# Kernel tuning notes

Hardware: AMD Instinct MI355X
Metric: run time of the kernel (lower is better)

## Reference

```python
import jax, jax.numpy as jnp
import numpy as np

TAU = 100.0
EPS = 1e-6

def _norm(a):
    n = jnp.linalg.norm(a, axis=-1, keepdims=True)
    return a / jnp.maximum(n, EPS)

def setup_inputs() -> dict:
    key = jax.random.key(0)
    k1, k2, k3 = jax.random.split(key, 3)
    A, T, B, V, D = 64, 32, 64, 12, 512
    text_feat = jax.random.normal(k1, (A, T, D), dtype=jnp.float32)
    video_feat = jax.random.normal(k2, (B, V, D), dtype=jnp.float32)
    text_mask = jax.random.randint(k3, (A, T), 0, 2, dtype=jnp.int32)
    # guarantee at least one valid token per text so masked softmaxes are finite
    text_mask = text_mask.at[:, 0].set(1)
    return {"text_feat": text_feat, "video_feat": video_feat, "text_mask": text_mask}

def reference(text_feat, video_feat, text_mask):
    tm = text_mask.astype(text_feat.dtype)          # [A,T]
    t = _norm(text_feat)                            # [A,T,D]
    v = _norm(video_feat)                           # [B,V,D]
    neg_inf = jnp.asarray(-jnp.inf, t.dtype)

    logits = jnp.einsum('atd,bvd->abtv', t, v)      # [A,B,T,V]
    logits = logits * tm[:, None, :, None]          # zero out masked text tokens

    # video-side softmax over frames v, then aggregate video into text space
    vps1 = jax.nn.softmax(logits * TAU, axis=-1)            # [A,B,T,V]
    tf1 = jnp.einsum('abtv,bvd->abtd', vps1, v)             # [A,B,T,D]  (largest intermediate)
    t2v = jnp.einsum('abtd,atd->abt', tf1, t)               # [A,B,T]

    # text-side masked softmax over tokens t, aggregate text into video space
    tps1 = jax.nn.softmax(jnp.where(logits == 0, neg_inf, logits) * TAU, axis=-2)
    vf1 = jnp.einsum('abtv,atd->abvd', tps1, t)             # [A,B,V,D]
    v2t = jnp.einsum('abvd,bvd->abv', vf1, v)               # [A,B,V]

    tps2 = jax.nn.softmax(jnp.where(t2v == 0, neg_inf, t2v) * TAU, axis=-1)
    vf2 = jnp.einsum('abt,atd->abd', tps2, t)               # [A,B,D]
    vps2 = jax.nn.softmax(v2t * TAU, axis=-1)
    tf2 = jnp.einsum('abv,bvd->abd', vps2, v)               # [A,B,D]

    return jnp.einsum('abd,abd->ab', vf2, tf2)              # [A,B]
```

## Files before the change

kernel.cpp:

```cpp
#include <hip/hip_runtime.h>
#include <math.h>

#define A_ 64
#define T_ 32
#define B_ 64
#define V_ 12
#define D_ 512
#define TAUF 100.0f
#define NCH 8

#define AHI 0
#define ALO 8192
#define BHI 16384
#define BLO 22528
#define BUFBYTES 28672

typedef __attribute__((ext_vector_type(8))) short bf16x8;
typedef __attribute__((ext_vector_type(4))) float f32x4;

__device__ __forceinline__ void splitT(const float4 x0, const float4 x1,
                                       bf16x8& hv, bf16x8& lv, float& ss)
{
    float y[8] = {x0.x, x0.y, x0.z, x0.w, x1.x, x1.y, x1.z, x1.w};
    #pragma unroll
    for (int j = 0; j < 8; ++j) {
        ss += y[j] * y[j];
        unsigned int u = __float_as_uint(y[j]);
        float hf = __uint_as_float(u & 0xffff0000u);
        hv[j] = (short)(u >> 16);
        lv[j] = (short)(__float_as_uint(y[j] - hf) >> 16);
    }
}

__global__ __launch_bounds__(256)
void fused_kernel(const float* __restrict__ text,
                  const float* __restrict__ video,
                  const int* __restrict__ mask,
                  float* __restrict__ out)
{
    const int wgid = blockIdx.x;
    const int xcd  = wgid & 7;
    const int i    = wgid >> 3;
    const int bm   = xcd * 4 + (i >> 4);
    const int bn   = i & 15;
    const int tid  = threadIdx.x;
    const int wid  = tid >> 6;
    const int lane = tid & 63;
    const int r16  = lane & 15;
    const int kg4  = lane >> 4;

    __shared__ __align__(16) char stage[2][BUFBYTES];
    __shared__ float nrmA[8][64];
    __shared__ float nrmB[8][48];
    __shared__ float invA[64];
    __shared__ float invB[48];
    __shared__ int   msh[2][T_];
    __shared__ float v2t_sh[8][V_];
    __shared__ float wv_sh[8][V_];
    __shared__ float stats1[8];

    if (tid < 64) msh[tid >> 5][tid & 31] = mask[(bm * 2 + (tid >> 5)) * T_ + (tid & 31)];

    const int arow0 = tid >> 3, akg = tid & 7;
    const int arow1 = arow0 + 32;
    const float* asrc0 = text + ((size_t)(bm * 64 + arow0)) * D_ + akg * 8;
    const float* asrc1 = text + ((size_t)(bm * 64 + arow1)) * D_ + akg * 8;
    const int brow0 = tid >> 3, bkg = tid & 7;
    const int brow1 = brow0 + 24;
    const float* bsrc0 = video + ((size_t)(bn * 48 + brow0)) * D_ + bkg * 8;
    const float* bsrc1 = video + ((size_t)(bn * 48 + brow1)) * D_ + bkg * 8;

    const int adst0 = (akg * 64 + (arow0 ^ akg)) * 16;
    const int adst1 = (akg * 64 + (arow1 ^ akg)) * 16;
    const int bdst0 = BHI + (bkg * 48 + (brow0 ^ bkg)) * 16;
    const int bdst1 = BHI + (bkg * 48 + (brow1 ^ bkg)) * 16;

    float ssA0 = 0.f, ssA1 = 0.f, ssB0 = 0.f, ssB1 = 0.f;

    auto PACK = [&](int bufi, int k) {
        char* buf = stage[bufi];
        {
            const float4* s = (const float4*)(asrc0 + k * 64);
            bf16x8 hv, lv;
            splitT(s[0], s[1], hv, lv, ssA0);
            *(bf16x8*)(buf + adst0)       = hv;
            *(bf16x8*)(buf + ALO + adst0) = lv;
        }
        {
            const float4* s = (const float4*)(asrc1 + k * 64);
            bf16x8 hv, lv;
            splitT(s[0], s[1], hv, lv, ssA1);
            *(bf16x8*)(buf + adst1)       = hv;
            *(bf16x8*)(buf + ALO + adst1) = lv;
        }
        if (tid < 192) {
            {
                const float4* s = (const float4*)(bsrc0 + k * 64);
                bf16x8 hv, lv;
                splitT(s[0], s[1], hv, lv, ssB0);
                *(bf16x8*)(buf + bdst0)             = hv;
                *(bf16x8*)(buf + (BLO - BHI) + bdst0) = lv;
            }
            {
                const float4* s = (const float4*)(bsrc1 + k * 64);
                bf16x8 hv, lv;
                splitT(s[0], s[1], hv, lv, ssB1);
                *(bf16x8*)(buf + bdst1)             = hv;
                *(bf16x8*)(buf + (BLO - BHI) + bdst1) = lv;
            }
        }
    };

    const int rowa = wid * 16 + r16;
    int aoff[2], boff[2][3];
    #pragma unroll
    for (int s = 0; s < 2; ++s) {
        int kg = s * 4 + kg4;
        aoff[s] = (kg * 64 + (rowa ^ kg)) * 16;
        #pragma unroll
        for (int c = 0; c < 3; ++c) {
            int rowb = c * 16 + r16;
            boff[s][c] = BHI + (kg * 48 + (rowb ^ kg)) * 16;
        }
    }

    f32x4 acc0 = {0.f, 0.f, 0.f, 0.f};
    f32x4 acc1 = {0.f, 0.f, 0.f, 0.f};
    f32x4 acc2 = {0.f, 0.f, 0.f, 0.f};

    PACK(0, 0);
    __syncthreads();

    #pragma unroll 2
    for (int k = 0; k < NCH; ++k) {
        if (k + 1 < NCH) PACK((k + 1) & 1, k + 1);
        const char* buf = stage[k & 1];
        #pragma unroll
        for (int s = 0; s < 2; ++s) {
            bf16x8 aH  = *(const bf16x8*)(buf + aoff[s]);
            bf16x8 aL  = *(const bf16x8*)(buf + ALO + aoff[s]);
            bf16x8 bH0 = *(const bf16x8*)(buf + boff[s][0]);
            bf16x8 bL0 = *(const bf16x8*)(buf + (BLO - BHI) + boff[s][0]);
            bf16x8 bH1 = *(const bf16x8*)(buf + boff[s][1]);
            bf16x8 bL1 = *(const bf16x8*)(buf + (BLO - BHI) + boff[s][1]);
            bf16x8 bH2 = *(const bf16x8*)(buf + boff[s][2]);
            bf16x8 bL2 = *(const bf16x8*)(buf + (BLO - BHI) + boff[s][2]);
            acc0 = __builtin_amdgcn_mfma_f32_16x16x32_bf16(aH, bH0, acc0, 0, 0, 0);
            acc1 = __builtin_amdgcn_mfma_f32_16x16x32_bf16(aH, bH1, acc1, 0, 0, 0);
            acc2 = __builtin_amdgcn_mfma_f32_16x16x32_bf16(aH, bH2, acc2, 0, 0, 0);
            acc0 = __builtin_amdgcn_mfma_f32_16x16x32_bf16(aH, bL0, acc0, 0, 0, 0);
            acc1 = __builtin_amdgcn_mfma_f32_16x16x32_bf16(aH, bL1, acc1, 0, 0, 0);
            acc2 = __builtin_amdgcn_mfma_f32_16x16x32_bf16(aH, bL2, acc2, 0, 0, 0);
            acc0 = __builtin_amdgcn_mfma_f32_16x16x32_bf16(aL, bH0, acc0, 0, 0, 0);
            acc1 = __builtin_amdgcn_mfma_f32_16x16x32_bf16(aL, bH1, acc1, 0, 0, 0);
            acc2 = __builtin_amdgcn_mfma_f32_16x16x32_bf16(aL, bH2, acc2, 0, 0, 0);
        }
        __syncthreads();
    }

    nrmA[akg][arow0] = ssA0;
    nrmA[akg][arow1] = ssA1;
    if (tid < 192) { nrmB[bkg][brow0] = ssB0; nrmB[bkg][brow1] = ssB1; }
    __syncthreads();
    if (tid < 64) {
        float s = 0.f;
        #pragma unroll
        for (int j = 0; j < 8; ++j) s += nrmA[j][tid];
        invA[tid] = 1.0f / fmaxf(sqrtf(s), 1e-6f);
    } else if (tid < 112) {
        int r = tid - 64;
        float s = 0.f;
        #pragma unroll
        for (int j = 0; j < 8; ++j) s += nrmB[j][r];
        invB[r] = 1.0f / fmaxf(sqrtf(s), 1e-6f);
    }
    __syncthreads();

    float* Lf = (float*)&stage[0][0];
    {
        #pragma unroll
        for (int r = 0; r < 4; ++r) {
            int Mrow0 = wid * 16 + kg4 * 4 + r;
            int al = Mrow0 >> 5, t = Mrow0 & 31;
            float ia = invA[Mrow0];
            int c0 = r16, c1 = 16 + r16, c2 = 32 + r16;
            int bl0 = c0 / 12, bl1 = c1 / 12, bl2 = c2 / 12;
            Lf[((al * 4 + bl0) * T_ + t) * V_ + (c0 - bl0 * 12)] = acc0[r] * ia * invB[c0];
            Lf[((al * 4 + bl1) * T_ + t) * V_ + (c1 - bl1 * 12)] = acc1[r] * ia * invB[c1];
            Lf[((al * 4 + bl2) * T_ + t) * V_ + (c2 - bl2 * 12)] = acc2[r] * ia * invB[c2];
        }
    }
    __syncthreads();

    const int p   = tid >> 5;
    const int l32 = tid & 31;
    const int al  = p >> 2, bl = p & 3;
    const float* Lrow = &Lf[((al * 4 + bl) * T_ + l32) * V_];

    float t2v_val;
    {
        float l[V_];
        #pragma unroll
        for (int j = 0; j < V_; ++j) l[j] = Lrow[j];
        if (msh[al][l32]) {
            float m = -1e30f;
            #pragma unroll
            for (int j = 0; j < V_; ++j) m = fmaxf(m, l[j]);
            float s = 0.f, num = 0.f;
            #pragma unroll
            for (int j = 0; j < V_; ++j) {
                float e = expf(TAUF * (l[j] - m));
                s += e; num += e * l[j];
            }
            t2v_val = num / s;
        } else {
            float s = 0.f;
            #pragma unroll
            for (int j = 0; j < V_; ++j) s += l[j];
            t2v_val = s * (1.0f / V_);
        }
    }

    bool  ex = (t2v_val == 0.0f);
    float xm = ex ? -1e30f : t2v_val;
    #pragma unroll
    for (int m = 16; m >= 1; m >>= 1) xm = fmaxf(xm, __shfl_xor(xm, m, 32));
    float w2 = ex ? 0.0f : expf(TAUF * (t2v_val - xm));
    float W2 = w2;
    #pragma unroll
    for (int m = 16; m >= 1; m >>= 1) W2 += __shfl_xor(W2, m, 32);

    if (l32 < V_) {
        float m = -1e30f;
        for (int j = 0; j < T_; ++j) {
            float Lraw = Lf[((al * 4 + bl) * T_ + j) * V_ + l32];
            float Lm = msh[al][j] ? Lraw : 0.0f;
            if (Lm != 0.0f) m = fmaxf(m, Lm);
        }
        float s = 0.f, num = 0.f;
        for (int j = 0; j < T_; ++j) {
            float Lraw = Lf[((al * 4 + bl) * T_ + j) * V_ + l32];
            float Lm = msh[al][j] ? Lraw : 0.0f;
            if (Lm != 0.0f) {
                float e = expf(TAUF * (Lm - m));
                s += e; num += e * Lraw;
            }
        }
        v2t_sh[p][l32] = num / s;
    }
    __syncthreads();

    if (l32 < V_) {
        float m = -1e30f;
        #pragma unroll
        for (int j = 0; j < V_; ++j) m = fmaxf(m, v2t_sh[p][j]);
        float s = 0.f;
        #pragma unroll
        for (int j = 0; j < V_; ++j) s += expf(TAUF * (v2t_sh[p][j] - m));
        wv_sh[p][l32] = expf(TAUF * (v2t_sh[p][l32] - m));
        if (l32 == 0) stats1[p] = s;
    }
    __syncthreads();

    {
        float pD = 0.f;
        #pragma unroll
        for (int j = 0; j < V_; ++j) pD += wv_sh[p][j] * Lrow[j];
        pD *= w2;
        #pragma unroll
        for (int m = 16; m >= 1; m >>= 1) pD += __shfl_xor(pD, m, 32);
        if (l32 == 0)
            out[(bm * 2 + al) * B_ + bn * 4 + bl] = pD / (W2 * stats1[p]);
    }
}

extern "C" void kernel_launch(void* const* d_in, const int* in_sizes, int n_in,
                              void* d_out, int out_size, void* d_ws, size_t ws_size,
                              hipStream_t stream) {
    const float* text  = (const float*)d_in[0];
    const float* video = (const float*)d_in[1];
    const int*   mask  = (const int*)d_in[2];
    float* out = (float*)d_out;

    fused_kernel<<<512, 256, 0, stream>>>(text, video, mask, out);
}
```

Before: 20.69 us.

## Pre-pack bf16 hi/lo splits in separate kernel and stream B via global_load_lds

```diff
diff --git a/kernel.cpp b/kernel.cpp
--- a/kernel.cpp
+++ b/kernel.cpp
@@ -9,11 +9,10 @@
 #define TAUF 100.0f
 #define NCH 8
 
-#define AHI 0
-#define ALO 8192
-#define BHI 16384
-#define BLO 22528
-#define BUFBYTES 28672
+#define APAN_USH 65536
+#define ACH_USH  8192
+#define BPAN_USH 49152
+#define BCH_USH  6144
 
 typedef __attribute__((ext_vector_type(8))) short bf16x8;
 typedef __attribute__((ext_vector_type(4))) float f32x4;
@@ -33,8 +32,80 @@
 }
 
 __global__ __launch_bounds__(256)
-void fused_kernel(const float* __restrict__ text,
-                  const float* __restrict__ video,
+void pack_kernel(const float* __restrict__ text,
+                 const float* __restrict__ video,
+                 unsigned short* __restrict__ Apk,
+                 unsigned short* __restrict__ Bpk,
+                 float* __restrict__ Ans,
+                 float* __restrict__ Bns)
+{
+    const int blk = blockIdx.x;
+    const int tid = threadIdx.x;
+    const int row = tid >> 3, kg = tid & 7;
+
+    if (blk < 256) {
+        const int p = blk >> 3, k = blk & 7;
+        __shared__ float ps[64][8];
+        unsigned short* dst = Apk + (size_t)p * APAN_USH + k * ACH_USH;
+        float ss0 = 0.f, ss1 = 0.f;
+        {
+            const float4* s = (const float4*)(text + ((size_t)(p * 64 + row)) * D_ + k * 64 + kg * 8);
+            bf16x8 hv, lv; splitT(s[0], s[1], hv, lv, ss0);
+            *(bf16x8*)(dst + (kg * 64 + row) * 8)        = hv;
+            *(bf16x8*)(dst + 4096 + (kg * 64 + row) * 8) = lv;
+        }
+        {
+            const int r1 = row + 32;
+            const float4* s = (const float4*)(text + ((size_t)(p * 64 + r1)) * D_ + k * 64 + kg * 8);
+            bf16x8 hv, lv; splitT(s[0], s[1], hv, lv, ss1);
+            *(bf16x8*)(dst + (kg * 64 + r1) * 8)        = hv;
+            *(bf16x8*)(dst + 4096 + (kg * 64 + r1) * 8) = lv;
+        }
+        ps[row][kg] = ss0;
+        ps[row + 32][kg] = ss1;
+        __syncthreads();
+        if (tid < 64) {
+            float s = 0.f;
+            #pragma unroll
+            for (int j = 0; j < 8; ++j) s += ps[tid][j];
+            Ans[(p * 8 + k) * 64 + tid] = s;
+        }
+    } else {
+        const int j2 = blk - 256;
+        const int p = j2 >> 3, k = j2 & 7;
+        __shared__ float ps[48][8];
+        unsigned short* dst = Bpk + (size_t)p * BPAN_USH + k * BCH_USH;
+        float ss0 = 0.f, ss1 = 0.f;
+        {
+            const float4* s = (const float4*)(video + ((size_t)(p * 48 + row)) * D_ + k * 64 + kg * 8);
+            bf16x8 hv, lv; splitT(s[0], s[1], hv, lv, ss0);
+            *(bf16x8*)(dst + (kg * 48 + row) * 8)        = hv;
+            *(bf16x8*)(dst + 3072 + (kg * 48 + row) * 8) = lv;
+            ps[row][kg] = ss0;
+        }
+        if (tid < 128) {
+            const int r1 = row + 32;
+            const float4* s = (const float4*)(video + ((size_t)(p * 48 + r1)) * D_ + k * 64 + kg * 8);
+            bf16x8 hv, lv; splitT(s[0], s[1], hv, lv, ss1);
+            *(bf16x8*)(dst + (kg * 48 + r1) * 8)        = hv;
+            *(bf16x8*)(dst + 3072 + (kg * 48 + r1) * 8) = lv;
+            ps[r1][kg] = ss1;
+        }
+        __syncthreads();
+        if (tid < 48) {
+            float s = 0.f;
+            #pragma unroll
+            for (int j = 0; j < 8; ++j) s += ps[tid][j];
+            Bns[(p * 8 + k) * 48 + tid] = s;
+        }
+    }
+}
+
+__global__ __launch_bounds__(256)
+void fused_kernel(const unsigned short* __restrict__ Apk,
+                  const unsigned short* __restrict__ Bpk,
+                  const float* __restrict__ Ans,
+                  const float* __restrict__ Bns,
                   const int* __restrict__ mask,
                   float* __restrict__ out)
 {
@@ -49,9 +120,7 @@
     const int r16  = lane & 15;
     const int kg4  = lane >> 4;
 
-    __shared__ __align__(16) char stage[2][BUFBYTES];
-    __shared__ float nrmA[8][64];
-    __shared__ float nrmB[8][48];
+    __shared__ __align__(16) char stage[2][12288];
     __shared__ float invA[64];
     __shared__ float invB[48];
     __shared__ int   msh[2][T_];
@@ -61,90 +130,69 @@
 
     if (tid < 64) msh[tid >> 5][tid & 31] = mask[(bm * 2 + (tid >> 5)) * T_ + (tid & 31)];
 
-    const int arow0 = tid >> 3, akg = tid & 7;
-    const int arow1 = arow0 + 32;
-    const float* asrc0 = text + ((size_t)(bm * 64 + arow0)) * D_ + akg * 8;
-    const float* asrc1 = text + ((size_t)(bm * 64 + arow1)) * D_ + akg * 8;
-    const int brow0 = tid >> 3, bkg = tid & 7;
-    const int brow1 = brow0 + 24;
-    const float* bsrc0 = video + ((size_t)(bn * 48 + brow0)) * D_ + bkg * 8;
-    const float* bsrc1 = video + ((size_t)(bn * 48 + brow1)) * D_ + bkg * 8;
-
-    const int adst0 = (akg * 64 + (arow0 ^ akg)) * 16;
-    const int adst1 = (akg * 64 + (arow1 ^ akg)) * 16;
-    const int bdst0 = BHI + (bkg * 48 + (brow0 ^ bkg)) * 16;
-    const int bdst1 = BHI + (bkg * 48 + (brow1 ^ bkg)) * 16;
-
-    float ssA0 = 0.f, ssA1 = 0.f, ssB0 = 0.f, ssB1 = 0.f;
-
-    auto PACK = [&](int bufi, int k) {
-        char* buf = stage[bufi];
-        {
-            const float4* s = (const float4*)(asrc0 + k * 64);
-            bf16x8 hv, lv;
-            splitT(s[0], s[1], hv, lv, ssA0);
-            *(bf16x8*)(buf + adst0)       = hv;
-            *(bf16x8*)(buf + ALO + adst0) = lv;
-        }
-        {
-            const float4* s = (const float4*)(asrc1 + k * 64);
-            bf16x8 hv, lv;
-            splitT(s[0], s[1], hv, lv, ssA1);
-            *(bf16x8*)(buf + adst1)       = hv;
-            *(bf16x8*)(buf + ALO + adst1) = lv;
-        }
-        if (tid < 192) {
-            {
-                const float4* s = (const float4*)(bsrc0 + k * 64);
-                bf16x8 hv, lv;
-                splitT(s[0], s[1], hv, lv, ssB0);
-                *(bf16x8*)(buf + bdst0)             = hv;
-                *(bf16x8*)(buf + (BLO - BHI) + bdst0) = lv;
-            }
-            {
-                const float4* s = (const float4*)(bsrc1 + k * 64);
-                bf16x8 hv, lv;
-                splitT(s[0], s[1], hv, lv, ssB1);
-                *(bf16x8*)(buf + bdst1)             = hv;
-                *(bf16x8*)(buf + (BLO - BHI) + bdst1) = lv;
-            }
-        }
-    };
-
-    const int rowa = wid * 16 + r16;
-    int aoff[2], boff[2][3];
-    #pragma unroll
-    for (int s = 0; s < 2; ++s) {
-        int kg = s * 4 + kg4;
-        aoff[s] = (kg * 64 + (rowa ^ kg)) * 16;
-        #pragma unroll
-        for (int c = 0; c < 3; ++c) {
-            int rowb = c * 16 + r16;
-            boff[s][c] = BHI + (kg * 48 + (rowb ^ kg)) * 16;
-        }
-    }
+    const unsigned short* Abase = Apk + (size_t)bm * APAN_USH;
+    const unsigned short* Bbase = Bpk + (size_t)bn * BPAN_USH;
+
+    const int rowA  = wid * 16 + r16;
+    const int aoff0 = ((0 * 4 + kg4) * 64 + rowA) * 8;
+    const int aoff1 = ((1 * 4 + kg4) * 64 + rowA) * 8;
+
+    bf16x8 cH0, cH1, cL0, cL1;
+    bf16x8 nH0, nH1, nL0, nL1;
+
+    #define LOADA(k, H0, H1, L0, L1) do {                          \
+        const unsigned short* c_ = Abase + (k) * ACH_USH;          \
+        H0 = *(const bf16x8*)(c_ + aoff0);                         \
+        H1 = *(const bf16x8*)(c_ + aoff1);                         \
+        L0 = *(const bf16x8*)(c_ + 4096 + aoff0);                  \
+        L1 = *(const bf16x8*)(c_ + 4096 + aoff1);                  \
+    } while (0)
+
+    #define GLD16(srcp, dstp)                                      \
+        __builtin_amdgcn_global_load_lds(                          \
+            (const __attribute__((address_space(1))) unsigned int*)(srcp), \
+            (__attribute__((address_space(3))) unsigned int*)(dstp), 16, 0, 0)
+
+    #define STAGEB(bufi, k) do {                                   \
+        const unsigned short* c_ = Bbase + (k) * BCH_USH + wid * 512 + lane * 8; \
+        char* d_ = &stage[bufi][wid * 1024];                       \
+        GLD16(c_,        d_);                                      \
+        GLD16(c_ + 2048, d_ + 4096);                               \
+        GLD16(c_ + 4096, d_ + 8192);                               \
+    } while (0)
+
+    int boff[2][3];
+    #pragma unroll
+    for (int s = 0; s < 2; ++s)
+        #pragma unroll
+        for (int c = 0; c < 3; ++c)
+            boff[s][c] = ((s * 4 + kg4) * 48 + c * 16 + r16) * 16;
 
     f32x4 acc0 = {0.f, 0.f, 0.f, 0.f};
     f32x4 acc1 = {0.f, 0.f, 0.f, 0.f};
     f32x4 acc2 = {0.f, 0.f, 0.f, 0.f};
 
-    PACK(0, 0);
-    __syncthreads();
-
-    #pragma unroll 2
+    STAGEB(0, 0);
+    LOADA(0, cH0, cH1, cL0, cL1);
+    __syncthreads();
+
+    #pragma unroll
     for (int k = 0; k < NCH; ++k) {
-        if (k + 1 < NCH) PACK((k + 1) & 1, k + 1);
+        if (k + 1 < NCH) {
+            STAGEB((k + 1) & 1, k + 1);
+            LOADA(k + 1, nH0, nH1, nL0, nL1);
+        }
         const char* buf = stage[k & 1];
         #pragma unroll
         for (int s = 0; s < 2; ++s) {
-            bf16x8 aH  = *(const bf16x8*)(buf + aoff[s]);
-            bf16x8 aL  = *(const bf16x8*)(buf + ALO + aoff[s]);
+            bf16x8 aH  = s ? cH1 : cH0;
+            bf16x8 aL  = s ? cL1 : cL0;
             bf16x8 bH0 = *(const bf16x8*)(buf + boff[s][0]);
-            bf16x8 bL0 = *(const bf16x8*)(buf + (BLO - BHI) + boff[s][0]);
+            bf16x8 bL0 = *(const bf16x8*)(buf + 6144 + boff[s][0]);
             bf16x8 bH1 = *(const bf16x8*)(buf + boff[s][1]);
-            bf16x8 bL1 = *(const bf16x8*)(buf + (BLO - BHI) + boff[s][1]);
+            bf16x8 bL1 = *(const bf16x8*)(buf + 6144 + boff[s][1]);
             bf16x8 bH2 = *(const bf16x8*)(buf + boff[s][2]);
-            bf16x8 bL2 = *(const bf16x8*)(buf + (BLO - BHI) + boff[s][2]);
+            bf16x8 bL2 = *(const bf16x8*)(buf + 6144 + boff[s][2]);
             acc0 = __builtin_amdgcn_mfma_f32_16x16x32_bf16(aH, bH0, acc0, 0, 0, 0);
             acc1 = __builtin_amdgcn_mfma_f32_16x16x32_bf16(aH, bH1, acc1, 0, 0, 0);
             acc2 = __builtin_amdgcn_mfma_f32_16x16x32_bf16(aH, bH2, acc2, 0, 0, 0);
@@ -155,23 +203,20 @@
             acc1 = __builtin_amdgcn_mfma_f32_16x16x32_bf16(aL, bH1, acc1, 0, 0, 0);
             acc2 = __builtin_amdgcn_mfma_f32_16x16x32_bf16(aL, bH2, acc2, 0, 0, 0);
         }
+        cH0 = nH0; cH1 = nH1; cL0 = nL0; cL1 = nL1;
         __syncthreads();
     }
 
-    nrmA[akg][arow0] = ssA0;
-    nrmA[akg][arow1] = ssA1;
-    if (tid < 192) { nrmB[bkg][brow0] = ssB0; nrmB[bkg][brow1] = ssB1; }
-    __syncthreads();
     if (tid < 64) {
         float s = 0.f;
         #pragma unroll
-        for (int j = 0; j < 8; ++j) s += nrmA[j][tid];
+        for (int j = 0; j < 8; ++j) s += Ans[(bm * 8 + j) * 64 + tid];
         invA[tid] = 1.0f / fmaxf(sqrtf(s), 1e-6f);
     } else if (tid < 112) {
         int r = tid - 64;
         float s = 0.f;
         #pragma unroll
-        for (int j = 0; j < 8; ++j) s += nrmB[j][r];
+        for (int j = 0; j < 8; ++j) s += Bns[(bn * 8 + j) * 48 + r];
         invB[r] = 1.0f / fmaxf(sqrtf(s), 1e-6f);
     }
     __syncthreads();
@@ -272,6 +317,9 @@
         if (l32 == 0)
             out[(bm * 2 + al) * B_ + bn * 4 + bl] = pD / (W2 * stats1[p]);
     }
+    #undef LOADA
+    #undef GLD16
+    #undef STAGEB
 }
 
 extern "C" void kernel_launch(void* const* d_in, const int* in_sizes, int n_in,
@@ -282,5 +330,11 @@
     const int*   mask  = (const int*)d_in[2];
     float* out = (float*)d_out;
 
-    fused_kernel<<<512, 256, 0, stream>>>(text, video, mask, out);
+    unsigned short* Apk = (unsigned short*)d_ws;
+    unsigned short* Bpk = Apk + (size_t)32 * APAN_USH;
+    float* Ans = (float*)(Bpk + (size_t)16 * BPAN_USH);
+    float* Bns = Ans + 32 * 8 * 64;
+
+    pack_kernel<<<384, 256, 0, stream>>>(text, video, Apk, Bpk, Ans, Bns);
+    fused_kernel<<<512, 256, 0, stream>>>(Apk, Bpk, Ans, Bns, mask, out);
 }
```

After: 23.57 us. +13.9%, slower.
